# Kernel optimization log

Hardware: AMD Instinct MI355X
Metric: run time of the kernel (lower is better)

The kernel has to match this reference:

```python
import jax, jax.numpy as jnp
import numpy as np

B, S, D_MODEL, FFN, P = 8, 4096, 256, 1024, 8
BLK = 256  # token block size for the max-plus reduction


def setup_inputs() -> dict:
    key = jax.random.key(0)
    ks = jax.random.split(key, 12)
    x = jax.random.normal(ks[0], (B, S, D_MODEL), jnp.float32)
    # TropicalLinear params (additive semiring weights -> small scale)
    Wt = 0.05 * jax.random.normal(ks[1], (FFN, D_MODEL), jnp.float32)
    bt = 0.05 * jax.random.normal(ks[2], (FFN,), jnp.float32)
    # LFDualActivation: per-channel piecewise-linear convex (max) and concave (min)
    # branches, blended by a per-channel sigmoid gate alpha ('blend' mode).
    sl_cvx = 1.0 + 0.1 * jax.random.normal(ks[3], (FFN, P), jnp.float32)
    of_cvx = 0.1 * jax.random.normal(ks[4], (FFN, P), jnp.float32)
    sl_ccv = 1.0 + 0.1 * jax.random.normal(ks[5], (FFN, P), jnp.float32)
    of_ccv = 0.1 * jax.random.normal(ks[6], (FFN, P), jnp.float32)
    alpha = jnp.zeros((FFN,), jnp.float32)
    # Classical branch
    Wc = jax.random.normal(ks[7], (D_MODEL, FFN), jnp.float32) / np.sqrt(D_MODEL)
    bc = jnp.zeros((FFN,), jnp.float32)
    # Gate: init per source (weight ~0, bias +2.0 -> g ~ 0.88 tropical)
    Wg = 0.01 * jax.random.normal(ks[8], (D_MODEL, FFN), jnp.float32)
    bg = 2.0 * jnp.ones((FFN,), jnp.float32)
    # Down projection
    Wd = jax.random.normal(ks[9], (FFN, D_MODEL), jnp.float32) / np.sqrt(FFN)
    bd = jnp.zeros((D_MODEL,), jnp.float32)
    return {"x": x, "Wt": Wt, "bt": bt, "sl_cvx": sl_cvx, "of_cvx": of_cvx,
            "sl_ccv": sl_ccv, "of_ccv": of_ccv, "alpha": alpha,
            "Wc": Wc, "bc": bc, "Wg": Wg, "bg": bg, "Wd": Wd, "bd": bd}


def reference(x, Wt, bt, sl_cvx, of_cvx, sl_ccv, of_ccv, alpha, Wc, bc, Wg, bg, Wd, bd):
    Bx, Sx, D = x.shape
    T = Bx * Sx
    xf = x.reshape(T, D)
    xb = xf.reshape(T // BLK, BLK, D)
    s = jax.nn.sigmoid(alpha)  # [FFN]

    def blk_fn(xx):  # xx: [BLK, D]
        # Tropical (max-plus) linear: t[n,m] = max_k(xx[n,k] + Wt[m,k]) + bt[m]
        t = jnp.max(xx[:, None, :] + Wt[None, :, :], axis=-1) + bt  # [BLK, FFN]
        # LF dual activation: blend of convex (max of lines) and concave (min of lines)
        z = t[:, :, None]  # [BLK, FFN, 1]
        cvx = jnp.max(z * sl_cvx[None] + of_cvx[None], axis=-1)
        ccv = jnp.min(z * sl_ccv[None] + of_ccv[None], axis=-1)
        return s * cvx + (1.0 - s) * ccv  # [BLK, FFN]

    trop = jax.lax.map(blk_fn, xb).reshape(T, FFN)  # dropout = identity (eval)
    classical = jax.nn.gelu(xf @ Wc + bc, approximate=False)
    g = jax.nn.sigmoid(xf @ Wg + bg)
    fused = g * trop + (1.0 - g) * classical
    out = fused @ Wd + bd  # final dropout = identity (eval)
    return out.reshape(Bx, Sx, D)
```

## Files before the change

kernel.cpp:

```cpp
#include <hip/hip_runtime.h>

#define TTOK 32768
#define DM   256
#define NF   1024
#define KMAX 32

typedef __attribute__((ext_vector_type(8))) unsigned short ushort8;
typedef __attribute__((ext_vector_type(8))) __bf16 bf16x8;
typedef __attribute__((ext_vector_type(4))) float floatx4;

constexpr size_t O_SLOT = 0;
constexpr size_t O_S    = 256;
constexpr size_t O_WCT  = O_S    + 4096;
constexpr size_t O_WGT  = O_WCT  + (size_t)NF*DM*2;
constexpr size_t O_WDT  = O_WGT  + (size_t)NF*DM*2;
constexpr size_t O_WTT  = O_WDT  + (size_t)DM*NF*2;
constexpr size_t O_XBF  = O_WTT  + (size_t)DM*NF*4;
constexpr size_t O_CNT  = O_XBF  + (size_t)TTOK*DM*2;
constexpr size_t O_CIDX = O_CNT  + (size_t)TTOK*4;
constexpr size_t O_CVAL = O_CIDX + (size_t)TTOK*KMAX*4;
constexpr size_t O_FUSD = O_CVAL + (size_t)TTOK*KMAX*4;

__device__ __forceinline__ float bf2f(unsigned short u) {
    union { unsigned int i; float f; } c; c.i = ((unsigned int)u) << 16; return c.f;
}
__device__ __forceinline__ unsigned short f2bf(float v) {
    union { float f; unsigned int i; } c; c.f = v;
    unsigned int b = c.i;
    return (unsigned short)((b + 0x7FFFu + ((b >> 16) & 1u)) >> 16);
}
__device__ __forceinline__ float sigm(float z) { return 1.0f / (1.0f + __expf(-z)); }
__device__ __forceinline__ float gelu_f(float x) {
    return x * sigm(1.59576912f * (x + 0.044715f * x * x * x));
}
__device__ __forceinline__ void g2lds16(const unsigned short* g, unsigned short* l) {
    __builtin_amdgcn_global_load_lds((const __attribute__((address_space(1))) unsigned int*)g,
                                     (__attribute__((address_space(3))) unsigned int*)l, 16, 0, 0);
}

__global__ void pack_kernel(const float* __restrict__ Wt, const float* __restrict__ alpha,
                            const float* __restrict__ Wc, const float* __restrict__ Wg,
                            const float* __restrict__ Wd,
                            unsigned short* __restrict__ Wct, unsigned short* __restrict__ Wgt,
                            unsigned short* __restrict__ WdT, float* __restrict__ WtT,
                            float* __restrict__ s, unsigned int* __restrict__ slot) {
    int e = blockIdx.x * 256 + threadIdx.x;
    if (e == 0) *slot = 0u;
    { int f = e >> 8, k = e & 255;
      Wct[e] = f2bf(Wc[k * NF + f]);
      Wgt[e] = f2bf(Wg[k * NF + f]); }
    { int n = e >> 10, k = e & 1023;
      WdT[e] = f2bf(Wd[k * DM + n]); }
    { int d = e >> 10, f = e & 1023;
      WtT[e] = Wt[f * DM + d]; }
    if (e < NF) s[e] = sigm(alpha[e]);
}

__global__ void minmax_kernel(const float* __restrict__ Wt, unsigned int* __restrict__ slot) {
    int g = blockIdx.x * 256 + threadIdx.x;
    float lm = 0.0f;
    for (int i = g; i < NF * DM; i += 128 * 256) lm = fmaxf(lm, fabsf(Wt[i]));
    #pragma unroll
    for (int o = 32; o > 0; o >>= 1) lm = fmaxf(lm, __shfl_xor(lm, o));
    if ((threadIdx.x & 63) == 0) atomicMax(slot, __float_as_uint(lm));
}

__global__ void cand_kernel(const float* __restrict__ x, const unsigned int* __restrict__ slot,
                            unsigned short* __restrict__ xbf, int* __restrict__ counts,
                            int* __restrict__ cidx, float* __restrict__ cval) {
    int i = blockIdx.x, t = threadIdx.x;
    float v = x[i * DM + t];
    xbf[i * DM + t] = f2bf(v);
    float m = v;
    #pragma unroll
    for (int o = 32; o > 0; o >>= 1) m = fmaxf(m, __shfl_xor(m, o));
    __shared__ float wm[4];
    __shared__ int cnt;
    __shared__ int sidx[KMAX];
    __shared__ float sval[KMAX];
    if ((t & 63) == 0) wm[t >> 6] = m;
    if (t == 0) cnt = 0;
    __syncthreads();
    float xmax = fmaxf(fmaxf(wm[0], wm[1]), fmaxf(wm[2], wm[3]));
    float delta = 2.0f * __uint_as_float(*slot);
    float thr = xmax - delta;
    if (v >= thr) {
        int p = atomicAdd(&cnt, 1);
        if (p < KMAX) { sidx[p] = t; sval[p] = v; }
    }
    __syncthreads();
    int c = cnt;
    if (t == 0) counts[i] = c;
    if (t < (c < KMAX ? c : KMAX)) {
        cidx[i * KMAX + t] = sidx[t];
        cval[i * KMAX + t] = sval[t];
    }
}

#define LDSS 32
#define KPAD 33
#define OSTR 136
__global__ __launch_bounds__(512, 4) void gemm1_kernel(
    const unsigned short* __restrict__ A,
    const unsigned short* __restrict__ Bct,
    const unsigned short* __restrict__ Bgt,
    const float* __restrict__ bc, const float* __restrict__ bg,
    const int* __restrict__ counts, const int* __restrict__ cidx,
    const float* __restrict__ cval, const float* __restrict__ x,
    const float* __restrict__ WtT, const float* __restrict__ bt,
    const float* __restrict__ slx, const float* __restrict__ ofx,
    const float* __restrict__ slc, const float* __restrict__ ofc,
    const float* __restrict__ s, unsigned short* __restrict__ fused) {
    __shared__ __align__(16) char smem[76800];
    unsigned short* As  = (unsigned short*)smem;
    unsigned short* Bcs = As + 4096;
    unsigned short* Bgs = As + 8192;
    float* par = (float*)smem;
    int* sOV  = (int*)(smem + 24576);
    int* sCnt = (int*)(smem + 41472);
    unsigned short* obuf = (unsigned short*)(smem + 41984);
    const int t = threadIdx.x;
    const int b = blockIdx.x;
    const int xcd = b & 7, j = b >> 3;
    const int bf = j & 7;
    const int bm = (j >> 3) * 8 + xcd;
    const int wave = t >> 6, lane = t & 63;
    const int wm = wave & 1, wn = wave >> 1;
    const int lr = lane & 15, quad = lane >> 4;
    const int srow = wave * 16 + (lane >> 2), scol = (lane & 3) << 3;
    const unsigned short* gA = A   + (size_t)(bm * 128 + srow) * DM + scol;
    const unsigned short* gC = Bct + (size_t)(bf * 128 + srow) * DM + scol;
    const unsigned short* gG = Bgt + (size_t)(bf * 128 + srow) * DM + scol;
    unsigned short* lA = &As[wave * 16 * LDSS];
    unsigned short* lC = &Bcs[wave * 16 * LDSS];
    unsigned short* lG = &Bgs[wave * 16 * LDSS];

    if (t < 128) sCnt[t] = counts[bm * 128 + t];

    floatx4 accc[4][2], accg[4][2];
    #pragma unroll
    for (int i = 0; i < 4; i++)
        #pragma unroll
        for (int jj = 0; jj < 2; jj++) { accc[i][jj] = (floatx4)0.0f; accg[i][jj] = (floatx4)0.0f; }

    for (int k0 = 0; k0 < DM; k0 += 32) {
        __syncthreads();
        g2lds16(gA + k0, lA);
        g2lds16(gC + k0, lC);
        g2lds16(gG + k0, lG);
        __syncthreads();
        bf16x8 af[4], bcf[2], bgf[2];
        #pragma unroll
        for (int mi = 0; mi < 4; mi++)
            af[mi] = *(const bf16x8*)&As[(wm * 64 + mi * 16 + lr) * LDSS + quad * 8];
        #pragma unroll
        for (int ni = 0; ni < 2; ni++) {
            bcf[ni] = *(const bf16x8*)&Bcs[(wn * 32 + ni * 16 + lr) * LDSS + quad * 8];
            bgf[ni] = *(const bf16x8*)&Bgs[(wn * 32 + ni * 16 + lr) * LDSS + quad * 8];
        }
        #pragma unroll
        for (int mi = 0; mi < 4; mi++)
            #pragma unroll
            for (int ni = 0; ni < 2; ni++) {
                accc[mi][ni] = __builtin_amdgcn_mfma_f32_16x16x32_bf16(af[mi], bcf[ni], accc[mi][ni], 0, 0, 0);
                accg[mi][ni] = __builtin_amdgcn_mfma_f32_16x16x32_bf16(af[mi], bgf[ni], accg[mi][ni], 0, 0, 0);
            }
    }
    __syncthreads();

    for (int e = t; e < 1024; e += 512) {
        int ff = e >> 3, w = e & 7;
        int gf = (bf * 128 + ff) * 8 + w;
        par[ff * 36 + w]      = slx[gf];
        par[ff * 36 + 8 + w]  = ofx[gf];
        par[ff * 36 + 16 + w] = slc[gf];
        par[ff * 36 + 24 + w] = ofc[gf];
    }
    if (t < 128) {
        int gf = bf * 128 + t;
        par[t * 36 + 32] = bt[gf];
        par[t * 36 + 33] = s[gf];
        par[t * 36 + 34] = bc[gf];
        par[t * 36 + 35] = bg[gf];
    }
    const int PADV = (int)(((unsigned int)f2bf(-1e30f)) << 16);
    for (int e = t; e < 128 * KMAX; e += 512) {
        int m = e >> 5, k = e & 31;
        int c = sCnt[m];
        int pk = PADV;
        if (k < (c < KMAX ? c : KMAX)) {
            int d  = cidx[(size_t)(bm * 128 + m) * KMAX + k];
            float v = cval[(size_t)(bm * 128 + m) * KMAX + k];
            pk = (int)(((unsigned int)f2bf(v)) << 16) | d;
        }
        sOV[m * KPAD + k] = pk;
    }
    __syncthreads();

    const int f0 = bf * 128 + wn * 32 + lr;
    #pragma unroll
    for (int mi = 0; mi < 4; mi++) {
        const int mb = wm * 64 + mi * 16 + quad * 4;
        int c0 = sCnt[mb], c1 = sCnt[mb + 1], c2 = sCnt[mb + 2], c3 = sCnt[mb + 3];
        int k0c = c0 < KMAX ? c0 : KMAX, k1c = c1 < KMAX ? c1 : KMAX;
        int k2c = c2 < KMAX ? c2 : KMAX, k3c = c3 < KMAX ? c3 : KMAX;
        int km = max(max(k0c, k1c), max(k2c, k3c));
        float z0a = -1e30f, z1a = -1e30f, z2a = -1e30f, z3a = -1e30f;
        float z0b = -1e30f, z1b = -1e30f, z2b = -1e30f, z3b = -1e30f;
        for (int k = 0; k < km; k++) {
            int p0 = sOV[(mb + 0) * KPAD + k];
            int p1 = sOV[(mb + 1) * KPAD + k];
            int p2 = sOV[(mb + 2) * KPAD + k];
            int p3 = sOV[(mb + 3) * KPAD + k];
            const float* r0 = WtT + ((p0 & 0xFFFF) << 10) + f0;
            const float* r1 = WtT + ((p1 & 0xFFFF) << 10) + f0;
            const float* r2 = WtT + ((p2 & 0xFFFF) << 10) + f0;
            const float* r3 = WtT + ((p3 & 0xFFFF) << 10) + f0;
            float w0a = r0[0], w0b = r0[16];
            float w1a = r1[0], w1b = r1[16];
            float w2a = r2[0], w2b = r2[16];
            float w3a = r3[0], w3b = r3[16];
            float v0 = __int_as_float(p0 & 0xFFFF0000);
            float v1 = __int_as_float(p1 & 0xFFFF0000);
            float v2 = __int_as_float(p2 & 0xFFFF0000);
            float v3 = __int_as_float(p3 & 0xFFFF0000);
            z0a = fmaxf(z0a, v0 + w0a); z0b = fmaxf(z0b, v0 + w0b);
            z1a = fmaxf(z1a, v1 + w1a); z1b = fmaxf(z1b, v1 + w1b);
            z2a = fmaxf(z2a, v2 + w2a); z2b = fmaxf(z2b, v2 + w2b);
            z3a = fmaxf(z3a, v3 + w3a); z3b = fmaxf(z3b, v3 + w3b);
        }
        if (c0 > KMAX || c1 > KMAX || c2 > KMAX || c3 > KMAX) {
            float za[4] = { z0a, z1a, z2a, z3a };
            float zb[4] = { z0b, z1b, z2b, z3b };
            int cc[4] = { c0, c1, c2, c3 };
            #pragma unroll 1
            for (int r = 0; r < 4; r++) if (cc[r] > KMAX) {
                const float* xr = x + (size_t)(bm * 128 + mb + r) * DM;
                float ma = -1e30f, mbv = -1e30f;
                for (int d = 0; d < DM; d++) {
                    float xv = xr[d];
                    ma  = fmaxf(ma,  xv + WtT[d * NF + f0]);
                    mbv = fmaxf(mbv, xv + WtT[d * NF + f0 + 16]);
                }
                za[r] = ma; zb[r] = mbv;
            }
            z0a = za[0]; z1a = za[1]; z2a = za[2]; z3a = za[3];
            z0b = zb[0]; z1b = zb[1]; z2b = zb[2]; z3b = zb[3];
        }
        #pragma unroll
        for (int ni = 0; ni < 2; ni++) {
            const int fl = wn * 32 + ni * 16 + lr;
            const float* pp = par + fl * 36;
            float4 a0 = *(const float4*)(pp),      a1 = *(const float4*)(pp + 4);
            float4 b0 = *(const float4*)(pp + 8),  b1 = *(const float4*)(pp + 12);
            float4 cc0 = *(const float4*)(pp + 16), cc1 = *(const float4*)(pp + 20);
            float4 d0 = *(const float4*)(pp + 24), d1 = *(const float4*)(pp + 28);
            float4 sc = *(const float4*)(pp + 32);
            float zr[4];
            if (ni == 0) { zr[0] = z0a; zr[1] = z1a; zr[2] = z2a; zr[3] = z3a; }
            else         { zr[0] = z0b; zr[1] = z1b; zr[2] = z2b; zr[3] = z3b; }
            #pragma unroll
            for (int r = 0; r < 4; r++) {
                float z = zr[r] + sc.x;
                float cvx = fmaf(z, a0.x, b0.x);
                cvx = fmaxf(cvx, fmaf(z, a0.y, b0.y));
                cvx = fmaxf(cvx, fmaf(z, a0.z, b0.z));
                cvx = fmaxf(cvx, fmaf(z, a0.w, b0.w));
                cvx = fmaxf(cvx, fmaf(z, a1.x, b1.x));
                cvx = fmaxf(cvx, fmaf(z, a1.y, b1.y));
                cvx = fmaxf(cvx, fmaf(z, a1.z, b1.z));
                cvx = fmaxf(cvx, fmaf(z, a1.w, b1.w));
                float ccv = fmaf(z, cc0.x, d0.x);
                ccv = fminf(ccv, fmaf(z, cc0.y, d0.y));
                ccv = fminf(ccv, fmaf(z, cc0.z, d0.z));
                ccv = fminf(ccv, fmaf(z, cc0.w, d0.w));
                ccv = fminf(ccv, fmaf(z, cc1.x, d1.x));
                ccv = fminf(ccv, fmaf(z, cc1.y, d1.y));
                ccv = fminf(ccv, fmaf(z, cc1.z, d1.z));
                ccv = fminf(ccv, fmaf(z, cc1.w, d1.w));
                float tv = sc.y * cvx + (1.0f - sc.y) * ccv;
                float cpre = accc[mi][ni][r] + sc.z;
                float gpre = accg[mi][ni][r] + sc.w;
                float g = sigm(gpre);
                float cla = gelu_f(cpre);
                obuf[(mb + r) * OSTR + fl] = f2bf(g * tv + (1.0f - g) * cla);
            }
        }
    }
    __syncthreads();
    #pragma unroll
    for (int e = t; e < 128 * 16; e += 512) {
        int row = e >> 4, c8 = (e & 15) << 3;
        ushort8 v = *(const ushort8*)&obuf[row * OSTR + c8];
        *(ushort8*)&fused[(size_t)(bm * 128 + row) * NF + bf * 128 + c8] = v;
    }
}

#define LDS2 64
__global__ __launch_bounds__(512, 4) void gemm2_kernel(
    const unsigned short* __restrict__ A,
    const unsigned short* __restrict__ Bt,
    const float* __restrict__ bd, float* __restrict__ out) {
    __shared__ __align__(16) unsigned short As[128 * LDS2];
    __shared__ __align__(16) unsigned short Bs[128 * LDS2];
    const int t = threadIdx.x;
    const int b = blockIdx.x;
    const int xcd = b & 7, j = b >> 3;
    const int bn = j & 1;
    const int bm = (j >> 1) * 8 + xcd;
    const int wave = t >> 6, lane = t & 63;
    const int wm = wave & 1, wn = wave >> 1;
    const int lr = lane & 15, quad = lane >> 4;
    const int srow = wave * 8 + (lane >> 3), scol = (lane & 7) << 3;
    const unsigned short* gA = A  + (size_t)(bm * 128 + srow) * NF + scol;
    const unsigned short* gB = Bt + (size_t)(bn * 128 + srow) * NF + scol;
    unsigned short* lA = &As[wave * 8 * LDS2];
    unsigned short* lB = &Bs[wave * 8 * LDS2];

    floatx4 acc[4][2];
    #pragma unroll
    for (int i = 0; i < 4; i++)
        #pragma unroll
        for (int jj = 0; jj < 2; jj++) acc[i][jj] = (floatx4)0.0f;

    for (int k0 = 0; k0 < NF; k0 += 64) {
        __syncthreads();
        g2lds16(gA + k0, lA);
        g2lds16(gA + k0 + (size_t)64 * NF, lA + 64 * LDS2);
        g2lds16(gB + k0, lB);
        g2lds16(gB + k0 + (size_t)64 * NF, lB + 64 * LDS2);
        __syncthreads();
        #pragma unroll
        for (int ks = 0; ks < 2; ks++) {
            bf16x8 af[4], bf_[2];
            #pragma unroll
            for (int mi = 0; mi < 4; mi++)
                af[mi] = *(const bf16x8*)&As[(wm * 64 + mi * 16 + lr) * LDS2 + ks * 32 + quad * 8];
            #pragma unroll
            for (int ni = 0; ni < 2; ni++)
                bf_[ni] = *(const bf16x8*)&Bs[(wn * 32 + ni * 16 + lr) * LDS2 + ks * 32 + quad * 8];
            #pragma unroll
            for (int mi = 0; mi < 4; mi++)
                #pragma unroll
                for (int ni = 0; ni < 2; ni++)
                    acc[mi][ni] = __builtin_amdgcn_mfma_f32_16x16x32_bf16(af[mi], bf_[ni], acc[mi][ni], 0, 0, 0);
        }
    }
    #pragma unroll
    for (int mi = 0; mi < 4; mi++)
        #pragma unroll
        for (int ni = 0; ni < 2; ni++) {
            int n = bn * 128 + wn * 32 + ni * 16 + lr;
            float bdv = bd[n];
            #pragma unroll
            for (int r = 0; r < 4; r++) {
                int m = bm * 128 + wm * 64 + mi * 16 + quad * 4 + r;
                out[m * DM + n] = acc[mi][ni][r] + bdv;
            }
        }
}

extern "C" void kernel_launch(void* const* d_in, const int* in_sizes, int n_in,
                              void* d_out, int out_size, void* d_ws, size_t ws_size,
                              hipStream_t stream) {
    const float* x     = (const float*)d_in[0];
    const float* Wt    = (const float*)d_in[1];
    const float* bt    = (const float*)d_in[2];
    const float* slx   = (const float*)d_in[3];
    const float* ofx   = (const float*)d_in[4];
    const float* slc   = (const float*)d_in[5];
    const float* ofc   = (const float*)d_in[6];
    const float* alpha = (const float*)d_in[7];
    const float* Wc    = (const float*)d_in[8];
    const float* bc    = (const float*)d_in[9];
    const float* Wg    = (const float*)d_in[10];
    const float* bg    = (const float*)d_in[11];
    const float* Wd    = (const float*)d_in[12];
    const float* bd    = (const float*)d_in[13];
    float* out = (float*)d_out;
    char* ws = (char*)d_ws;

    unsigned int* slot = (unsigned int*)(ws + O_SLOT);
    float* s           = (float*)(ws + O_S);
    unsigned short* Wct = (unsigned short*)(ws + O_WCT);
    unsigned short* Wgt = (unsigned short*)(ws + O_WGT);
    unsigned short* WdT = (unsigned short*)(ws + O_WDT);
    float* WtT          = (float*)(ws + O_WTT);
    unsigned short* xbf = (unsigned short*)(ws + O_XBF);
    int* counts         = (int*)(ws + O_CNT);
    int* cidx           = (int*)(ws + O_CIDX);
    float* cval         = (float*)(ws + O_CVAL);
    unsigned short* fused = (unsigned short*)(ws + O_FUSD);

    pack_kernel<<<1024, 256, 0, stream>>>(Wt, alpha, Wc, Wg, Wd, Wct, Wgt, WdT, WtT, s, slot);
    minmax_kernel<<<128, 256, 0, stream>>>(Wt, slot);
    cand_kernel<<<TTOK, 256, 0, stream>>>(x, slot, xbf, counts, cidx, cval);
    gemm1_kernel<<<2048, 512, 0, stream>>>(
        xbf, Wct, Wgt, bc, bg, counts, cidx, cval, x, WtT, bt,
        slx, ofx, slc, ofc, s, fused);
    gemm2_kernel<<<512, 512, 0, stream>>>(fused, WdT, bd, out);
}
```

Before: 285.4 us.

## Restructure candidate selection per-wave and tropical gather per-row with packed activations

The candidate kernel now handles one token per wave instead of one per 256-thread block. It uses float4 loads and ballot/popcount compaction, which removes the shared-memory atomics and block barriers. In gemm1 the max-plus gather is remapped so each wave handles 16 full rows across all 128 features, removing the per-quad max-count divergence. Results are staged as packed bf16 pairs in LDS, and the activation epilogue uses two-wide float vectors over the feature pairs, written out in two halves. The trade-offs are an extra LDS round trip, bf16 rounding of the tropical pre-activation, and more barriers.

```diff
diff --git a/kernel.cpp b/kernel.cpp
--- a/kernel.cpp
+++ b/kernel.cpp
@@ -8,6 +8,7 @@
 typedef __attribute__((ext_vector_type(8))) unsigned short ushort8;
 typedef __attribute__((ext_vector_type(8))) __bf16 bf16x8;
 typedef __attribute__((ext_vector_type(4))) float floatx4;
+typedef __attribute__((ext_vector_type(2))) float f32x2;
 
 constexpr size_t O_SLOT = 0;
 constexpr size_t O_S    = 256;
@@ -68,33 +69,33 @@
 __global__ void cand_kernel(const float* __restrict__ x, const unsigned int* __restrict__ slot,
                             unsigned short* __restrict__ xbf, int* __restrict__ counts,
                             int* __restrict__ cidx, float* __restrict__ cval) {
-    int i = blockIdx.x, t = threadIdx.x;
-    float v = x[i * DM + t];
-    xbf[i * DM + t] = f2bf(v);
-    float m = v;
+    const int wave = threadIdx.x >> 6, lane = threadIdx.x & 63;
+    const int i = blockIdx.x * 4 + wave;
+    float4 xv = *(const float4*)(x + (size_t)i * DM + lane * 4);
+    ushort4 xb;
+    xb.x = f2bf(xv.x); xb.y = f2bf(xv.y); xb.z = f2bf(xv.z); xb.w = f2bf(xv.w);
+    *(ushort4*)(xbf + (size_t)i * DM + lane * 4) = xb;
+    float m = fmaxf(fmaxf(xv.x, xv.y), fmaxf(xv.z, xv.w));
     #pragma unroll
     for (int o = 32; o > 0; o >>= 1) m = fmaxf(m, __shfl_xor(m, o));
-    __shared__ float wm[4];
-    __shared__ int cnt;
-    __shared__ int sidx[KMAX];
-    __shared__ float sval[KMAX];
-    if ((t & 63) == 0) wm[t >> 6] = m;
-    if (t == 0) cnt = 0;
-    __syncthreads();
-    float xmax = fmaxf(fmaxf(wm[0], wm[1]), fmaxf(wm[2], wm[3]));
     float delta = 2.0f * __uint_as_float(*slot);
-    float thr = xmax - delta;
-    if (v >= thr) {
-        int p = atomicAdd(&cnt, 1);
-        if (p < KMAX) { sidx[p] = t; sval[p] = v; }
-    }
-    __syncthreads();
-    int c = cnt;
-    if (t == 0) counts[i] = c;
-    if (t < (c < KMAX ? c : KMAX)) {
-        cidx[i * KMAX + t] = sidx[t];
-        cval[i * KMAX + t] = sval[t];
-    }
+    float thr = m - delta;
+    unsigned long long ltmask = (lane == 63) ? ~0ULL >> 1 : ((1ULL << (lane + (lane != 63))) - 1);
+    ltmask = (1ULL << lane) - 1;
+    int base = 0;
+    float vv[4] = { xv.x, xv.y, xv.z, xv.w };
+    #pragma unroll
+    for (int j = 0; j < 4; j++) {
+        bool p = vv[j] >= thr;
+        unsigned long long mk = __ballot(p);
+        int pos = base + (int)__popcll(mk & ltmask);
+        if (p && pos < KMAX) {
+            cidx[(size_t)i * KMAX + pos] = lane * 4 + j;
+            cval[(size_t)i * KMAX + pos] = vv[j];
+        }
+        base += (int)__popcll(mk);
+    }
+    if (lane == 0) counts[i] = base;
 }
 
 #define LDSS 32
@@ -111,14 +112,15 @@
     const float* __restrict__ slx, const float* __restrict__ ofx,
     const float* __restrict__ slc, const float* __restrict__ ofc,
     const float* __restrict__ s, unsigned short* __restrict__ fused) {
-    __shared__ __align__(16) char smem[76800];
+    __shared__ __align__(16) char smem[70144];
     unsigned short* As  = (unsigned short*)smem;
     unsigned short* Bcs = As + 4096;
     unsigned short* Bgs = As + 8192;
-    float* par = (float*)smem;
-    int* sOV  = (int*)(smem + 24576);
-    int* sCnt = (int*)(smem + 41472);
-    unsigned short* obuf = (unsigned short*)(smem + 41984);
+    unsigned int* zbuf = (unsigned int*)smem;
+    int* sCnt = (int*)(smem + 33280);
+    int* sOV  = (int*)(smem + 33792);
+    float* par2 = (float*)(smem + 33792);
+    unsigned short* obuf = (unsigned short*)(smem + 52736);
     const int t = threadIdx.x;
     const int b = blockIdx.x;
     const int xcd = b & 7, j = b >> 3;
@@ -168,21 +170,6 @@
     }
     __syncthreads();
 
-    for (int e = t; e < 1024; e += 512) {
-        int ff = e >> 3, w = e & 7;
-        int gf = (bf * 128 + ff) * 8 + w;
-        par[ff * 36 + w]      = slx[gf];
-        par[ff * 36 + 8 + w]  = ofx[gf];
-        par[ff * 36 + 16 + w] = slc[gf];
-        par[ff * 36 + 24 + w] = ofc[gf];
-    }
-    if (t < 128) {
-        int gf = bf * 128 + t;
-        par[t * 36 + 32] = bt[gf];
-        par[t * 36 + 33] = s[gf];
-        par[t * 36 + 34] = bc[gf];
-        par[t * 36 + 35] = bg[gf];
-    }
     const int PADV = (int)(((unsigned int)f2bf(-1e30f)) << 16);
     for (int e = t; e < 128 * KMAX; e += 512) {
         int m = e >> 5, k = e & 31;
@@ -197,102 +184,127 @@
     }
     __syncthreads();
 
-    const int f0 = bf * 128 + wn * 32 + lr;
-    #pragma unroll
-    for (int mi = 0; mi < 4; mi++) {
-        const int mb = wm * 64 + mi * 16 + quad * 4;
-        int c0 = sCnt[mb], c1 = sCnt[mb + 1], c2 = sCnt[mb + 2], c3 = sCnt[mb + 3];
-        int k0c = c0 < KMAX ? c0 : KMAX, k1c = c1 < KMAX ? c1 : KMAX;
-        int k2c = c2 < KMAX ? c2 : KMAX, k3c = c3 < KMAX ? c3 : KMAX;
-        int km = max(max(k0c, k1c), max(k2c, k3c));
-        float z0a = -1e30f, z1a = -1e30f, z2a = -1e30f, z3a = -1e30f;
-        float z0b = -1e30f, z1b = -1e30f, z2b = -1e30f, z3b = -1e30f;
-        for (int k = 0; k < km; k++) {
-            int p0 = sOV[(mb + 0) * KPAD + k];
-            int p1 = sOV[(mb + 1) * KPAD + k];
-            int p2 = sOV[(mb + 2) * KPAD + k];
-            int p3 = sOV[(mb + 3) * KPAD + k];
-            const float* r0 = WtT + ((p0 & 0xFFFF) << 10) + f0;
-            const float* r1 = WtT + ((p1 & 0xFFFF) << 10) + f0;
-            const float* r2 = WtT + ((p2 & 0xFFFF) << 10) + f0;
-            const float* r3 = WtT + ((p3 & 0xFFFF) << 10) + f0;
-            float w0a = r0[0], w0b = r0[16];
-            float w1a = r1[0], w1b = r1[16];
-            float w2a = r2[0], w2b = r2[16];
-            float w3a = r3[0], w3b = r3[16];
-            float v0 = __int_as_float(p0 & 0xFFFF0000);
-            float v1 = __int_as_float(p1 & 0xFFFF0000);
-            float v2 = __int_as_float(p2 & 0xFFFF0000);
-            float v3 = __int_as_float(p3 & 0xFFFF0000);
-            z0a = fmaxf(z0a, v0 + w0a); z0b = fmaxf(z0b, v0 + w0b);
-            z1a = fmaxf(z1a, v1 + w1a); z1b = fmaxf(z1b, v1 + w1b);
-            z2a = fmaxf(z2a, v2 + w2a); z2b = fmaxf(z2b, v2 + w2b);
-            z3a = fmaxf(z3a, v3 + w3a); z3b = fmaxf(z3b, v3 + w3b);
-        }
-        if (c0 > KMAX || c1 > KMAX || c2 > KMAX || c3 > KMAX) {
-            float za[4] = { z0a, z1a, z2a, z3a };
-            float zb[4] = { z0b, z1b, z2b, z3b };
-            int cc[4] = { c0, c1, c2, c3 };
-            #pragma unroll 1
-            for (int r = 0; r < 4; r++) if (cc[r] > KMAX) {
-                const float* xr = x + (size_t)(bm * 128 + mb + r) * DM;
-                float ma = -1e30f, mbv = -1e30f;
+    {
+        const int fa = bf * 128 + ((lane >> 4) * 32) + (lane & 15);
+        for (int mm = 0; mm < 16; mm++) {
+            int m = wave * 16 + mm;
+            int c = sCnt[m];
+            float za = -1e30f, zb = -1e30f;
+            if (c <= KMAX) {
+                int k = 0;
+                for (; k + 1 < c; k += 2) {
+                    int p0 = sOV[m * KPAD + k];
+                    int p1 = sOV[m * KPAD + k + 1];
+                    const float* r0 = WtT + ((p0 & 0xFFFF) << 10) + fa;
+                    const float* r1 = WtT + ((p1 & 0xFFFF) << 10) + fa;
+                    float w0a = r0[0], w0b = r0[16];
+                    float w1a = r1[0], w1b = r1[16];
+                    float v0 = __int_as_float(p0 & 0xFFFF0000);
+                    float v1 = __int_as_float(p1 & 0xFFFF0000);
+                    za = fmaxf(za, v0 + w0a); zb = fmaxf(zb, v0 + w0b);
+                    za = fmaxf(za, v1 + w1a); zb = fmaxf(zb, v1 + w1b);
+                }
+                if (k < c) {
+                    int p0 = sOV[m * KPAD + k];
+                    const float* r0 = WtT + ((p0 & 0xFFFF) << 10) + fa;
+                    float v0 = __int_as_float(p0 & 0xFFFF0000);
+                    za = fmaxf(za, v0 + r0[0]); zb = fmaxf(zb, v0 + r0[16]);
+                }
+            } else {
+                const float* xr = x + (size_t)(bm * 128 + m) * DM;
                 for (int d = 0; d < DM; d++) {
                     float xv = xr[d];
-                    ma  = fmaxf(ma,  xv + WtT[d * NF + f0]);
-                    mbv = fmaxf(mbv, xv + WtT[d * NF + f0 + 16]);
+                    const float* r0 = WtT + d * NF + fa;
+                    za = fmaxf(za, xv + r0[0]); zb = fmaxf(zb, xv + r0[16]);
                 }
-                za[r] = ma; zb[r] = mbv;
-            }
-            z0a = za[0]; z1a = za[1]; z2a = za[2]; z3a = za[3];
-            z0b = zb[0]; z1b = zb[1]; z2b = zb[2]; z3b = zb[3];
-        }
-        #pragma unroll
-        for (int ni = 0; ni < 2; ni++) {
-            const int fl = wn * 32 + ni * 16 + lr;
-            const float* pp = par + fl * 36;
-            float4 a0 = *(const float4*)(pp),      a1 = *(const float4*)(pp + 4);
-            float4 b0 = *(const float4*)(pp + 8),  b1 = *(const float4*)(pp + 12);
-            float4 cc0 = *(const float4*)(pp + 16), cc1 = *(const float4*)(pp + 20);
-            float4 d0 = *(const float4*)(pp + 24), d1 = *(const float4*)(pp + 28);
-            float4 sc = *(const float4*)(pp + 32);
-            float zr[4];
-            if (ni == 0) { zr[0] = z0a; zr[1] = z1a; zr[2] = z2a; zr[3] = z3a; }
-            else         { zr[0] = z0b; zr[1] = z1b; zr[2] = z2b; zr[3] = z3b; }
+            }
+            zbuf[m * 65 + lane] = ((unsigned int)f2bf(zb) << 16) | f2bf(za);
+        }
+    }
+    __syncthreads();
+
+    for (int e = t; e < 64 * 36; e += 512) {
+        int jl2 = e / 36, idx = e % 36;
+        int f0 = bf * 128 + ((jl2 >> 4) * 32) + (jl2 & 15);
+        float v0, v1;
+        if (idx < 8)       { v0 = slx[f0 * 8 + idx];      v1 = slx[(f0 + 16) * 8 + idx]; }
+        else if (idx < 16) { v0 = ofx[f0 * 8 + idx - 8];  v1 = ofx[(f0 + 16) * 8 + idx - 8]; }
+        else if (idx < 24) { v0 = slc[f0 * 8 + idx - 16]; v1 = slc[(f0 + 16) * 8 + idx - 16]; }
+        else if (idx < 32) { v0 = ofc[f0 * 8 + idx - 24]; v1 = ofc[(f0 + 16) * 8 + idx - 24]; }
+        else if (idx == 32){ v0 = bt[f0]; v1 = bt[f0 + 16]; }
+        else if (idx == 33){ v0 = s[f0];  v1 = s[f0 + 16]; }
+        else if (idx == 34){ v0 = bc[f0]; v1 = bc[f0 + 16]; }
+        else               { v0 = bg[f0]; v1 = bg[f0 + 16]; }
+        par2[jl2 * 74 + idx * 2]     = v0;
+        par2[jl2 * 74 + idx * 2 + 1] = v1;
+    }
+    __syncthreads();
+
+    const int jl = wn * 16 + lr;
+    const float* pp = par2 + jl * 74;
+    f32x2 bt2 = *(const f32x2*)(pp + 64);
+    f32x2 s2  = *(const f32x2*)(pp + 66);
+    f32x2 bc2 = *(const f32x2*)(pp + 68);
+    f32x2 bg2 = *(const f32x2*)(pp + 70);
+    for (int h = 0; h < 2; h++) {
+        #pragma unroll
+        for (int mi2 = 0; mi2 < 2; mi2++) {
+            const int mi = h * 2 + mi2;
+            const int mb = wm * 64 + mi * 16 + quad * 4;
+            f32x2 z2[4];
             #pragma unroll
             for (int r = 0; r < 4; r++) {
-                float z = zr[r] + sc.x;
-                float cvx = fmaf(z, a0.x, b0.x);
-                cvx = fmaxf(cvx, fmaf(z, a0.y, b0.y));
-                cvx = fmaxf(cvx, fmaf(z, a0.z, b0.z));
-                cvx = fmaxf(cvx, fmaf(z, a0.w, b0.w));
-                cvx = fmaxf(cvx, fmaf(z, a1.x, b1.x));
-                cvx = fmaxf(cvx, fmaf(z, a1.y, b1.y));
-                cvx = fmaxf(cvx, fmaf(z, a1.z, b1.z));
-                cvx = fmaxf(cvx, fmaf(z, a1.w, b1.w));
-                float ccv = fmaf(z, cc0.x, d0.x);
-                ccv = fminf(ccv, fmaf(z, cc0.y, d0.y));
-                ccv = fminf(ccv, fmaf(z, cc0.z, d0.z));
-                ccv = fminf(ccv, fmaf(z, cc0.w, d0.w));
-                ccv = fminf(ccv, fmaf(z, cc1.x, d1.x));
-                ccv = fminf(ccv, fmaf(z, cc1.y, d1.y));
-                ccv = fminf(ccv, fmaf(z, cc1.z, d1.z));
-                ccv = fminf(ccv, fmaf(z, cc1.w, d1.w));
-                float tv = sc.y * cvx + (1.0f - sc.y) * ccv;
-                float cpre = accc[mi][ni][r] + sc.z;
-                float gpre = accg[mi][ni][r] + sc.w;
-                float g = sigm(gpre);
-                float cla = gelu_f(cpre);
-                obuf[(mb + r) * OSTR + fl] = f2bf(g * tv + (1.0f - g) * cla);
-            }
-        }
-    }
-    __syncthreads();
-    #pragma unroll
-    for (int e = t; e < 128 * 16; e += 512) {
-        int row = e >> 4, c8 = (e & 15) << 3;
-        ushort8 v = *(const ushort8*)&obuf[row * OSTR + c8];
-        *(ushort8*)&fused[(size_t)(bm * 128 + row) * NF + bf * 128 + c8] = v;
+                unsigned int u = zbuf[(mb + r) * 65 + jl];
+                f32x2 zz;
+                zz.x = bf2f((unsigned short)(u & 0xFFFF));
+                zz.y = bf2f((unsigned short)(u >> 16));
+                z2[r] = zz + bt2;
+            }
+            f32x2 cvx[4], ccv[4];
+            #pragma unroll
+            for (int r = 0; r < 4; r++)
+                cvx[r] = __builtin_elementwise_fma(z2[r], *(const f32x2*)(pp + 0), *(const f32x2*)(pp + 16));
+            #pragma unroll
+            for (int jj = 1; jj < 8; jj++) {
+                f32x2 sl = *(const f32x2*)(pp + 2 * jj);
+                f32x2 of = *(const f32x2*)(pp + 16 + 2 * jj);
+                #pragma unroll
+                for (int r = 0; r < 4; r++)
+                    cvx[r] = __builtin_elementwise_max(cvx[r], __builtin_elementwise_fma(z2[r], sl, of));
+            }
+            #pragma unroll
+            for (int r = 0; r < 4; r++)
+                ccv[r] = __builtin_elementwise_fma(z2[r], *(const f32x2*)(pp + 32), *(const f32x2*)(pp + 48));
+            #pragma unroll
+            for (int jj = 1; jj < 8; jj++) {
+                f32x2 sl = *(const f32x2*)(pp + 32 + 2 * jj);
+                f32x2 of = *(const f32x2*)(pp + 48 + 2 * jj);
+                #pragma unroll
+                for (int r = 0; r < 4; r++)
+                    ccv[r] = __builtin_elementwise_min(ccv[r], __builtin_elementwise_fma(z2[r], sl, of));
+            }
+            #pragma unroll
+            for (int r = 0; r < 4; r++) {
+                f32x2 tv = __builtin_elementwise_fma(s2, cvx[r] - ccv[r], ccv[r]);
+                f32x2 cpre; cpre.x = accc[mi][0][r]; cpre.y = accc[mi][1][r]; cpre += bc2;
+                f32x2 gpre; gpre.x = accg[mi][0][r]; gpre.y = accg[mi][1][r]; gpre += bg2;
+                float g0 = sigm(gpre.x), g1 = sigm(gpre.y);
+                float c0 = gelu_f(cpre.x), c1 = gelu_f(cpre.y);
+                float o0 = fmaf(g0, tv.x - c0, c0);
+                float o1 = fmaf(g1, tv.y - c1, c1);
+                int o = wm * 32 + mi2 * 16 + quad * 4 + r;
+                obuf[o * OSTR + wn * 32 + lr]      = f2bf(o0);
+                obuf[o * OSTR + wn * 32 + lr + 16] = f2bf(o1);
+            }
+        }
+        __syncthreads();
+        for (int e = t; e < 64 * 16; e += 512) {
+            int o = e >> 4, c8 = (e & 15) << 3;
+            ushort8 v = *(const ushort8*)&obuf[o * OSTR + c8];
+            int ml = (o >> 5) * 64 + h * 32 + (o & 31);
+            *(ushort8*)&fused[(size_t)(bm * 128 + ml) * NF + bf * 128 + c8] = v;
+        }
+        __syncthreads();
     }
 }
 
@@ -394,7 +406,7 @@
 
     pack_kernel<<<1024, 256, 0, stream>>>(Wt, alpha, Wc, Wg, Wd, Wct, Wgt, WdT, WtT, s, slot);
     minmax_kernel<<<128, 256, 0, stream>>>(Wt, slot);
-    cand_kernel<<<TTOK, 256, 0, stream>>>(x, slot, xbf, counts, cidx, cval);
+    cand_kernel<<<TTOK / 4, 256, 0, stream>>>(x, slot, xbf, counts, cidx, cval);
     gemm1_kernel<<<2048, 512, 0, stream>>>(
         xbf, Wct, Wgt, bc, bg, counts, cidx, cval, x, WtT, bt,
         slx, ofx, slc, ofc, s, fused);
```

After: 450.1 us. +57.7%, slower.
